# Optimization experiments

Hardware: AMD Instinct MI355X
Metric: run time of the kernel (lower is better)

The kernel has to match this reference:

```python
import jax, jax.numpy as jnp
import numpy as np

K = 29
NUM_CLASSES = 10
BN_EPS = 1e-5


def _conv_bn_relu(x, w, b, scale, bias, mean, var):
    # x: [B,C,H,W], w: [O,I,3,3], SAME padding, stride 1, eval-mode BN
    y = jax.lax.conv_general_dilated(x, w, (1, 1), 'SAME',
                                     dimension_numbers=('NCHW', 'OIHW', 'NCHW'))
    y = y + b[None, :, None, None]
    inv = jax.lax.rsqrt(var + BN_EPS)
    y = scale[None, :, None, None] * (y - mean[None, :, None, None]) * inv[None, :, None, None] \
        + bias[None, :, None, None]
    return jax.nn.relu(y)


def _maxpool2(x):
    return jax.lax.reduce_window(x, -jnp.inf, jax.lax.max,
                                 (1, 1, 2, 2), (1, 1, 2, 2), 'VALID')


def setup_inputs() -> dict:
    key = jax.random.key(0)
    ks = jax.random.split(key, 4)
    B, N, D = 64, 10000, 8192
    inp = {
        'imgs': jax.random.normal(ks[0], (B, 3, 32, 32), dtype=jnp.float32),
        'conv1_w': jax.random.normal(ks[1], (64, 3, 3, 3), dtype=jnp.float32) * 0.1,
        'conv1_b': jnp.zeros((64,), jnp.float32),
        'bn1_scale': jnp.ones((64,), jnp.float32),
        'bn1_bias': jnp.zeros((64,), jnp.float32),
        'bn1_mean': jnp.zeros((64,), jnp.float32),
        'bn1_var': jnp.ones((64,), jnp.float32),
        'conv2_w': jax.random.normal(ks[2], (128, 64, 3, 3), dtype=jnp.float32) * 0.05,
        'conv2_b': jnp.zeros((128,), jnp.float32),
        'bn2_scale': jnp.ones((128,), jnp.float32),
        'bn2_bias': jnp.zeros((128,), jnp.float32),
        'bn2_mean': jnp.zeros((128,), jnp.float32),
        'bn2_var': jnp.ones((128,), jnp.float32),
        'train_feats': jax.random.uniform(ks[3], (N, D), dtype=jnp.float32),
        'train_labels': jax.random.randint(jax.random.fold_in(key, 7), (N,), 0, NUM_CLASSES, dtype=jnp.int32),
    }
    return inp


def reference(imgs, conv1_w, conv1_b, bn1_scale, bn1_bias, bn1_mean, bn1_var,
              conv2_w, conv2_b, bn2_scale, bn2_bias, bn2_mean, bn2_var,
              train_feats, train_labels):
    # features[:layer_id+1] = conv-bn-relu, maxpool, conv-bn-relu, maxpool
    h = _conv_bn_relu(imgs, conv1_w, conv1_b, bn1_scale, bn1_bias, bn1_mean, bn1_var)
    h = _maxpool2(h)
    h = _conv_bn_relu(h, conv2_w, conv2_b, bn2_scale, bn2_bias, bn2_mean, bn2_var)
    h = _maxpool2(h)                             # [B,128,8,8]
    feats = h.reshape(h.shape[0], -1)            # [B, 8192]

    # L1 distances to the train bank, one test row at a time (avoids B*N*D blow-up,
    # mirrors the original per-image loop)
    def _row_dist(f):                            # f: [D] -> [N]
        return jnp.sum(jnp.abs(f[None, :] - train_feats), axis=-1)
    D_ij = jax.lax.map(_row_dist, feats)         # [B, N]

    neg_vals, inds = jax.lax.top_k(-D_ij, K)     # smallest K distances
    vals = -neg_vals                             # [B, K] L1 distances to neighbors

    # s = median of the K neighbor distances (detached in the original)
    s = jax.lax.stop_gradient(jnp.median(vals, axis=1))  # [B]

    lab_knn = train_labels[inds]                 # [B, K]
    counts = jnp.sum(jax.nn.one_hot(lab_knn, NUM_CLASSES, dtype=jnp.float32), axis=1)
    pred_cls = jnp.argmax(counts, axis=1)        # mode; ties -> smallest class (matches torch.mode)

    # exp-weighted density ratio; |x - nbr|_1 equals the topk distance itself
    w = jnp.exp(-vals / s[:, None])              # [B, K]
    mask = (lab_knn == pred_cls[:, None]).astype(w.dtype)
    nr = jnp.sum(w * mask, axis=1)
    dr = jnp.sum(w, axis=1)
    frac = nr / dr
    return jnp.stack([frac, 1.0 - frac], axis=1)  # [B, 2]
```

## Files before the change

### kernel.cpp

```cpp
#include <hip/hip_runtime.h>
#include <hip/hip_bf16.h>
#include <math.h>

#define BN_EPS 1e-5f
#define TOPK_K 29

__global__ __launch_bounds__(256) void conv1_kernel(
    const float* __restrict__ imgs, const float* __restrict__ w,
    const float* __restrict__ bconv, const float* __restrict__ scale,
    const float* __restrict__ bias, const float* __restrict__ mean,
    const float* __restrict__ var, float* __restrict__ p1)
{
    __shared__ float img_s[3][34][36];
    const int tid = (int)threadIdx.x;
    const int b = (int)blockIdx.y, ocg = (int)blockIdx.x;

    for (int i = tid; i < 3 * 34 * 36; i += 256) ((float*)img_s)[i] = 0.0f;
    __syncthreads();
    const float* ib = imgs + (size_t)b * 3 * 32 * 32;
    for (int i = tid; i < 3 * 32 * 32; i += 256) {
        int c = i >> 10, r = (i >> 5) & 31, x = i & 31;
        img_s[c][r + 1][x + 1] = ib[i];
    }
    __syncthreads();

    const int y = tid >> 4, x = tid & 15;
    float win[3][4][4];
#pragma unroll
    for (int c = 0; c < 3; ++c)
#pragma unroll
        for (int r = 0; r < 4; ++r)
#pragma unroll
            for (int cc = 0; cc < 4; ++cc)
                win[c][r][cc] = img_s[c][2 * y + r][2 * x + cc];

    for (int k = 0; k < 16; ++k) {
        const int oc = ocg * 16 + k;
        const float* wp = w + oc * 27;
        float p00 = 0.f, p01 = 0.f, p10 = 0.f, p11 = 0.f;
#pragma unroll
        for (int c = 0; c < 3; ++c)
#pragma unroll
            for (int ky = 0; ky < 3; ++ky)
#pragma unroll
                for (int kx = 0; kx < 3; ++kx) {
                    float wv = wp[(c * 3 + ky) * 3 + kx];
                    p00 += win[c][ky][kx] * wv;
                    p01 += win[c][ky][kx + 1] * wv;
                    p10 += win[c][ky + 1][kx] * wv;
                    p11 += win[c][ky + 1][kx + 1] * wv;
                }
        const float a = scale[oc] / sqrtf(var[oc] + BN_EPS);
        const float c0 = (bconv[oc] - mean[oc]) * a + bias[oc];
        float m = fmaxf(fmaxf(p00 * a + c0, p01 * a + c0),
                        fmaxf(p10 * a + c0, p11 * a + c0));
        m = fmaxf(m, 0.0f);
        p1[(((size_t)b * 64 + oc) * 16 + y) * 16 + x] = m;
    }
}

__global__ __launch_bounds__(256) void conv2_kernel(
    const float* __restrict__ p1, const float* __restrict__ w,
    const float* __restrict__ bconv, const float* __restrict__ scale,
    const float* __restrict__ bias, const float* __restrict__ mean,
    const float* __restrict__ var, float* __restrict__ feats)
{
    __shared__ float in_s[64][16][18];
    const int tid = (int)threadIdx.x;
    const int b = (int)blockIdx.y, ocg = (int)blockIdx.x;

    for (int i = tid; i < 64 * 16 * 18; i += 256) ((float*)in_s)[i] = 0.0f;
    __syncthreads();
    const float* pb = p1 + (size_t)b * 64 * 256;
    for (int i = tid; i < 64 * 256; i += 256) {
        int c = i >> 8, r = (i >> 4) & 15, x = i & 15;
        in_s[c][r][x + 1] = pb[i];
    }
    __syncthreads();

    const int pix = tid & 63;
    const int wv_id = __builtin_amdgcn_readfirstlane(tid >> 6);
    const int y = pix >> 3, x = pix & 7;

    float acc[4][4];
#pragma unroll
    for (int k = 0; k < 4; ++k)
#pragma unroll
        for (int p = 0; p < 4; ++p) acc[k][p] = 0.0f;

    for (int c = 0; c < 64; ++c) {
        float win[4][4];
#pragma unroll
        for (int r = 0; r < 4; ++r) {
            int row = 2 * y - 1 + r;
            bool ok = (row >= 0) && (row < 16);
            const float2* rp = (const float2*)&in_s[c][ok ? row : 0][2 * x];
            float2 v0 = rp[0], v1 = rp[1];
            win[r][0] = ok ? v0.x : 0.0f;
            win[r][1] = ok ? v0.y : 0.0f;
            win[r][2] = ok ? v1.x : 0.0f;
            win[r][3] = ok ? v1.y : 0.0f;
        }
#pragma unroll
        for (int k = 0; k < 4; ++k) {
            const int oc = ocg * 16 + wv_id * 4 + k;
            const float* wp = w + ((size_t)oc * 64 + c) * 9;
#pragma unroll
            for (int ky = 0; ky < 3; ++ky)
#pragma unroll
                for (int kx = 0; kx < 3; ++kx) {
                    float wv = wp[ky * 3 + kx];
                    acc[k][0] += win[ky][kx] * wv;
                    acc[k][1] += win[ky][kx + 1] * wv;
                    acc[k][2] += win[ky + 1][kx] * wv;
                    acc[k][3] += win[ky + 1][kx + 1] * wv;
                }
        }
    }

#pragma unroll
    for (int k = 0; k < 4; ++k) {
        const int oc = ocg * 16 + wv_id * 4 + k;
        const float a = scale[oc] / sqrtf(var[oc] + BN_EPS);
        const float c0 = (bconv[oc] - mean[oc]) * a + bias[oc];
        float m = fmaxf(fmaxf(acc[k][0] * a + c0, acc[k][1] * a + c0),
                        fmaxf(acc[k][2] * a + c0, acc[k][3] * a + c0));
        m = fmaxf(m, 0.0f);
        feats[(size_t)b * 8192 + oc * 64 + pix] = m;
    }
}

__global__ __launch_bounds__(256) void dist_kernel(
    const float* __restrict__ feats, const float* __restrict__ train,
    float* __restrict__ Dm)
{
    const int tid = (int)threadIdx.x;
    const int lane = tid & 63;
    const int wv = tid >> 6;
    const int bh = __builtin_amdgcn_readfirstlane(wv & 1);
    const int ng = __builtin_amdgcn_readfirstlane(wv >> 1);
    const int nbase = (int)blockIdx.x * 128 + ng * 64;
    const int seg = (int)blockIdx.y;
    const int n = nbase + lane;
    const int nc = (n < 10000) ? n : 9999;

    const float* trow = train + (size_t)nc * 8192 + seg * 256;
    const float* fbase = feats + (size_t)(bh * 32) * 8192 + seg * 256;

    float acc[32];
#pragma unroll
    for (int i = 0; i < 32; ++i) acc[i] = 0.0f;

    for (int chunk = 0; chunk < 8; ++chunk) {
        float4 t[8];
#pragma unroll
        for (int q = 0; q < 8; ++q)
            t[q] = *(const float4*)(trow + chunk * 32 + q * 4);
#pragma unroll
        for (int bb = 0; bb < 32; ++bb) {
            const float4* fp = (const float4*)(fbase + (size_t)bb * 8192 + chunk * 32);
            float s0 = 0.0f, s1 = 0.0f;
#pragma unroll
            for (int q = 0; q < 8; ++q) {
                float4 f = fp[q];
                s0 += fabsf(t[q].x - f.x);
                s1 += fabsf(t[q].y - f.y);
                s0 += fabsf(t[q].z - f.z);
                s1 += fabsf(t[q].w - f.w);
            }
            acc[bb] += s0 + s1;
        }
    }

    if (n < 10000) {
#pragma unroll
        for (int bb = 0; bb < 32; ++bb)
            atomicAdd(&Dm[(size_t)(bh * 32 + bb) * 10000 + n], acc[bb]);
    }
}

__global__ __launch_bounds__(256) void topk_kernel(
    const float* __restrict__ Dm, const int* __restrict__ labels,
    float* __restrict__ out)
{
    __shared__ float dv[10000];
    __shared__ float wv_s[4];
    __shared__ int wi_s[4];
    __shared__ int win_s;
    __shared__ float kv[TOPK_K];
    __shared__ int kidx[TOPK_K];

    const int b = (int)blockIdx.x, tid = (int)threadIdx.x;
    const int lane = tid & 63, wid = tid >> 6;
    const float* row = Dm + (size_t)b * 10000;

    for (int nn = tid; nn < 10000; nn += 256) dv[nn] = row[nn];
    __syncthreads();

    float m = INFINITY;
    int mi = 0x7fffffff;
    for (int nn = tid; nn < 10000; nn += 256) {
        float v = dv[nn];
        if (v < m) { m = v; mi = nn; }
    }

    for (int k = 0; k < TOPK_K; ++k) {
        float rv = m;
        int ri = mi;
#pragma unroll
        for (int s = 1; s < 64; s <<= 1) {
            float ov = __shfl_xor(rv, s, 64);
            int oi = __shfl_xor(ri, s, 64);
            if (ov < rv || (ov == rv && oi < ri)) { rv = ov; ri = oi; }
        }
        if (lane == 0) { wv_s[wid] = rv; wi_s[wid] = ri; }
        __syncthreads();
        if (tid == 0) {
            float bv = wv_s[0];
            int bi = wi_s[0];
            for (int q = 1; q < 4; ++q)
                if (wv_s[q] < bv || (wv_s[q] == bv && wi_s[q] < bi)) {
                    bv = wv_s[q]; bi = wi_s[q];
                }
            kv[k] = bv; kidx[k] = bi; win_s = bi;
            dv[bi] = INFINITY;
        }
        __syncthreads();
        const int wn = win_s;
        if ((wn & 255) == tid) {
            m = INFINITY; mi = 0x7fffffff;
            for (int nn = tid; nn < 10000; nn += 256) {
                float v = dv[nn];
                if (v < m) { m = v; mi = nn; }
            }
        }
    }

    if (tid == 0) {
        const float s = kv[14];
        int cnt[10];
        int lab[TOPK_K];
        for (int c = 0; c < 10; ++c) cnt[c] = 0;
        for (int k = 0; k < TOPK_K; ++k) {
            lab[k] = labels[kidx[k]];
            cnt[lab[k]]++;
        }
        int pred = 0, bestc = cnt[0];
        for (int c = 1; c < 10; ++c)
            if (cnt[c] > bestc) { bestc = cnt[c]; pred = c; }
        float nr = 0.0f, dr = 0.0f;
        for (int k = 0; k < TOPK_K; ++k) {
            float wgt = expf(-kv[k] / s);
            dr += wgt;
            if (lab[k] == pred) nr += wgt;
        }
        const float frac = nr / dr;
        out[b * 2 + 0] = frac;
        out[b * 2 + 1] = 1.0f - frac;
    }
}

extern "C" void kernel_launch(void* const* d_in, const int* in_sizes, int n_in,
                              void* d_out, int out_size, void* d_ws, size_t ws_size,
                              hipStream_t stream) {
    const float* imgs = (const float*)d_in[0];
    const float* c1w = (const float*)d_in[1];
    const float* c1b = (const float*)d_in[2];
    const float* bn1s = (const float*)d_in[3];
    const float* bn1b = (const float*)d_in[4];
    const float* bn1m = (const float*)d_in[5];
    const float* bn1v = (const float*)d_in[6];
    const float* c2w = (const float*)d_in[7];
    const float* c2b = (const float*)d_in[8];
    const float* bn2s = (const float*)d_in[9];
    const float* bn2b = (const float*)d_in[10];
    const float* bn2m = (const float*)d_in[11];
    const float* bn2v = (const float*)d_in[12];
    const float* train = (const float*)d_in[13];
    const int* labels = (const int*)d_in[14];
    float* out = (float*)d_out;

    char* ws = (char*)d_ws;
    float* p1 = (float*)(ws);
    float* feats = (float*)(ws + 4194304);
    float* Dm = (float*)(ws + 4194304 + 2097152);

    hipMemsetAsync(Dm, 0, (size_t)64 * 10000 * sizeof(float), stream);
    conv1_kernel<<<dim3(4, 64), 256, 0, stream>>>(imgs, c1w, c1b, bn1s, bn1b, bn1m, bn1v, p1);
    conv2_kernel<<<dim3(8, 64), 256, 0, stream>>>(p1, c2w, c2b, bn2s, bn2b, bn2m, bn2v, feats);
    dist_kernel<<<dim3(79, 32), 256, 0, stream>>>(feats, train, Dm);
    topk_kernel<<<64, 256, 0, stream>>>(Dm, labels, out);
}
```

Measured before the change: 1.040 ms.

## Tile L1 distance kernel with LDS double-buffering and 8x8 register blocking

Rewrites the distance kernel so that each block stages 256 train rows and all 64 feature rows into LDS in 16-wide chunks. The staging uses global_load_lds with a swizzled layout and double buffering. Each thread then computes an 8x8 register tile of batch-by-train distances, replacing per-lane row streaming where feature values were re-read from global memory for every train row. This raises arithmetic reuse per loaded byte and overlaps loads with compute. The costs are more LDS use, barriers every chunk, higher register pressure under a 3-blocks-per-SM bound, and a larger atomic epilogue.

```diff
diff --git a/kernel.cpp b/kernel.cpp
--- a/kernel.cpp
+++ b/kernel.cpp
@@ -4,6 +4,11 @@
 
 #define BN_EPS 1e-5f
 #define TOPK_K 29
+
+#define NSEG 32
+#define SEGD 256
+#define CHD  16
+#define NCH  (SEGD/CHD)
 
 __global__ __launch_bounds__(256) void conv1_kernel(
     const float* __restrict__ imgs, const float* __restrict__ w,
@@ -130,52 +135,91 @@
     }
 }
 
-__global__ __launch_bounds__(256) void dist_kernel(
+__global__ __launch_bounds__(256, 3) void dist_kernel(
     const float* __restrict__ feats, const float* __restrict__ train,
     float* __restrict__ Dm)
 {
+    __shared__ __align__(16) float tr_s[2][256][CHD];
+    __shared__ __align__(16) float ft_s[2][64][CHD];
+
     const int tid = (int)threadIdx.x;
+    const int w = __builtin_amdgcn_readfirstlane(tid >> 6);
     const int lane = tid & 63;
-    const int wv = tid >> 6;
-    const int bh = __builtin_amdgcn_readfirstlane(wv & 1);
-    const int ng = __builtin_amdgcn_readfirstlane(wv >> 1);
-    const int nbase = (int)blockIdx.x * 128 + ng * 64;
-    const int seg = (int)blockIdx.y;
-    const int n = nbase + lane;
-    const int nc = (n < 10000) ? n : 9999;
-
-    const float* trow = train + (size_t)nc * 8192 + seg * 256;
-    const float* fbase = feats + (size_t)(bh * 32) * 8192 + seg * 256;
-
-    float acc[32];
-#pragma unroll
-    for (int i = 0; i < 32; ++i) acc[i] = 0.0f;
-
-    for (int chunk = 0; chunk < 8; ++chunk) {
-        float4 t[8];
-#pragma unroll
-        for (int q = 0; q < 8; ++q)
-            t[q] = *(const float4*)(trow + chunk * 32 + q * 4);
-#pragma unroll
-        for (int bb = 0; bb < 32; ++bb) {
-            const float4* fp = (const float4*)(fbase + (size_t)bb * 8192 + chunk * 32);
-            float s0 = 0.0f, s1 = 0.0f;
-#pragma unroll
-            for (int q = 0; q < 8; ++q) {
-                float4 f = fp[q];
-                s0 += fabsf(t[q].x - f.x);
-                s1 += fabsf(t[q].y - f.y);
-                s0 += fabsf(t[q].z - f.z);
-                s1 += fabsf(t[q].w - f.w);
-            }
-            acc[bb] += s0 + s1;
-        }
-    }
-
-    if (n < 10000) {
-#pragma unroll
-        for (int bb = 0; bb < 32; ++bb)
-            atomicAdd(&Dm[(size_t)(bh * 32 + bb) * 10000 + n], acc[bb]);
+    const int bq = lane >> 3, nq = lane & 7;
+    const int n0 = (int)blockIdx.x * 256;
+    const int d0 = (int)blockIdx.y * SEGD;
+
+    const int srow = lane >> 2;
+    const int sunit = (lane & 3) ^ ((srow >> 1) & 3);
+
+    const int mskB = (bq >> 1) & 3;
+    const int mskN = (nq >> 1) & 3;
+
+    auto stage = [&](int buf, int ch) {
+        const int dbase = d0 + ch * CHD + sunit * 4;
+#pragma unroll
+        for (int it = 0; it < 4; ++it) {
+            int r = it * 64 + w * 16 + srow;
+            int gn = n0 + r; if (gn > 9999) gn = 9999;
+            const float* src = train + (size_t)gn * 8192 + dbase;
+            __builtin_amdgcn_global_load_lds(
+                (const __attribute__((address_space(1))) void*)src,
+                (__attribute__((address_space(3))) void*)&tr_s[buf][it * 64 + w * 16][0],
+                16, 0, 0);
+        }
+        {
+            int rb = w * 16 + srow;
+            const float* src = feats + (size_t)rb * 8192 + dbase;
+            __builtin_amdgcn_global_load_lds(
+                (const __attribute__((address_space(1))) void*)src,
+                (__attribute__((address_space(3))) void*)&ft_s[buf][w * 16][0],
+                16, 0, 0);
+        }
+    };
+
+    float acc[8][8];
+#pragma unroll
+    for (int k = 0; k < 8; ++k)
+#pragma unroll
+        for (int j = 0; j < 8; ++j) acc[k][j] = 0.0f;
+
+    stage(0, 0);
+    __syncthreads();
+
+#pragma unroll 1
+    for (int ch = 0; ch < NCH; ++ch) {
+        if (ch + 1 < NCH) stage((ch + 1) & 1, ch + 1);
+        const int buf = ch & 1;
+#pragma unroll
+        for (int s = 0; s < 4; ++s) {
+            float4 f[8], t[8];
+#pragma unroll
+            for (int k = 0; k < 8; ++k)
+                f[k] = *(const float4*)&ft_s[buf][bq + 8 * k][(s ^ mskB) * 4];
+#pragma unroll
+            for (int j = 0; j < 8; ++j)
+                t[j] = *(const float4*)&tr_s[buf][w * 64 + nq + 8 * j][(s ^ mskN) * 4];
+#pragma unroll
+            for (int k = 0; k < 8; ++k)
+#pragma unroll
+                for (int j = 0; j < 8; ++j) {
+                    acc[k][j] += fabsf(f[k].x - t[j].x);
+                    acc[k][j] += fabsf(f[k].y - t[j].y);
+                    acc[k][j] += fabsf(f[k].z - t[j].z);
+                    acc[k][j] += fabsf(f[k].w - t[j].w);
+                }
+        }
+        __syncthreads();
+    }
+
+#pragma unroll
+    for (int j = 0; j < 8; ++j) {
+        const int n = n0 + w * 64 + nq + 8 * j;
+        if (n < 10000) {
+#pragma unroll
+            for (int k = 0; k < 8; ++k)
+                atomicAdd(&Dm[(size_t)(bq + 8 * k) * 10000 + n], acc[k][j]);
+        }
     }
 }
 
@@ -288,6 +332,6 @@
     hipMemsetAsync(Dm, 0, (size_t)64 * 10000 * sizeof(float), stream);
     conv1_kernel<<<dim3(4, 64), 256, 0, stream>>>(imgs, c1w, c1b, bn1s, bn1b, bn1m, bn1v, p1);
     conv2_kernel<<<dim3(8, 64), 256, 0, stream>>>(p1, c2w, c2b, bn2s, bn2b, bn2m, bn2v, feats);
-    dist_kernel<<<dim3(79, 32), 256, 0, stream>>>(feats, train, Dm);
+    dist_kernel<<<dim3(40, NSEG), 256, 0, stream>>>(feats, train, Dm);
     topk_kernel<<<64, 256, 0, stream>>>(Dm, labels, out);
 }
```

Result: slower. 2.007 ms (+92.9%).
